# Kernel tuning notes

Hardware: AMD Instinct MI355X
Metric: run time of the kernel (lower is better)

The kernel has to match this reference:

```python
import jax, jax.numpy as jnp
import numpy as np

# Bipartite frontier sizes per layer (targets of layer i): fanouts [15,10,5] over 1024 seeds
N_TGT = (60000, 6000, 1024)


def sage_layer(x_src, n_tgt, src, dst, Wl, Wr, b):
    # PyG SAGEConv, aggr='mean', root_weight=True:
    #   out = lin_l(mean_{j in N(i)} x_j) + lin_r(x_i) + bias
    x_tgt = x_src[:n_tgt]                       # [n_tgt, d]
    msg = x_src[src]                            # gather: [E, d]
    agg = jax.ops.segment_sum(msg, dst, num_segments=n_tgt)
    cnt = jax.ops.segment_sum(jnp.ones((src.shape[0], 1), x_src.dtype), dst, num_segments=n_tgt)
    mean = agg / jnp.maximum(cnt, 1.0)          # zero-degree nodes -> 0
    return mean @ Wl + x_tgt @ Wr + b


def setup_inputs() -> dict:
    key = jax.random.key(0)
    ks = jax.random.split(key, 16)
    N0 = 900000
    E = (900000, 60000, 5120)
    dims = [(100, 256), (256, 256), (256, 47)]
    inp = {"x": jax.random.normal(ks[0], (N0, 100), dtype=jnp.float32)}
    n_src = (N0,) + N_TGT[:2]
    for i in range(3):
        inp[f"src{i}"] = jax.random.randint(ks[1 + 2 * i], (E[i],), 0, n_src[i])
        inp[f"dst{i}"] = jax.random.randint(ks[2 + 2 * i], (E[i],), 0, N_TGT[i])
    for i, (din, dout) in enumerate(dims):
        inp[f"Wl{i}"] = jax.random.normal(ks[7 + 3 * i], (din, dout), dtype=jnp.float32) * 0.05
        inp[f"Wr{i}"] = jax.random.normal(ks[8 + 3 * i], (din, dout), dtype=jnp.float32) * 0.05
        inp[f"b{i}"] = jnp.zeros((dout,), dtype=jnp.float32)
    return inp


def reference(x, src0, dst0, src1, dst1, src2, dst2,
              Wl0, Wr0, b0, Wl1, Wr1, b1, Wl2, Wr2, b2):
    srcs = (src0, src1, src2)
    dsts = (dst0, dst1, dst2)
    Wls = (Wl0, Wl1, Wl2)
    Wrs = (Wr0, Wr1, Wr2)
    bs = (b0, b1, b2)
    for i in range(3):
        x = sage_layer(x, N_TGT[i], srcs[i], dsts[i], Wls[i], Wrs[i], bs[i])
        if i != 2:
            x = jax.nn.relu(x)  # dropout is identity in eval mode
    return jax.nn.log_softmax(x, axis=-1)
```

## Files before the change

kernel.cpp:

```cpp
#include <hip/hip_runtime.h>
#include <hip/hip_bf16.h>


typedef short bf16x8 __attribute__((ext_vector_type(8)));
typedef float f32x4 __attribute__((ext_vector_type(4)));

static __device__ __forceinline__ unsigned short f2bf(float f) {
  unsigned u = __float_as_uint(f);
  unsigned r = u + 0x7FFFu + ((u >> 16) & 1u);
  return (unsigned short)(r >> 16);
}
static __device__ __forceinline__ float bf2f_lo(unsigned u) {
  return __uint_as_float(u << 16);
}
static __device__ __forceinline__ float bf2f_hi(unsigned u) {
  return __uint_as_float(u & 0xFFFF0000u);
}
static __device__ __forceinline__ unsigned packbf(float lo, float hi) {
  return ((unsigned)f2bf(hi) << 16) | (unsigned)f2bf(lo);
}

#define E0C 900000
#define E1C 60000
#define E2C 5120
#define ETC 965120
#define HB  3770

#define ROW0_OFF 0
#define ROW1_OFF 60001
#define ROW2_OFF 66002
#define CNT_OFF  67027
#define RANK_OFF 134051
#define SS0_OFF  1099171
#define SS1_OFF  1999171
#define SS2_OFF  2059171

struct TileGeom { int tin, goff, n, T; };
static __device__ __forceinline__ TileGeom tile_geom(int b) {
  TileGeom g;
  if (b < 118)      { g.tin = b;       g.goff = 0;     g.n = 60000; g.T = 118; }
  else if (b < 130) { g.tin = b - 118; g.goff = 60000; g.n = 6000;  g.T = 12; }
  else              { g.tin = b - 130; g.goff = 66000; g.n = 1024;  g.T = 2; }
  return g;
}

__global__ __launch_bounds__(256) void histrank_k(
    const int* __restrict__ d0, const int* __restrict__ d1, const int* __restrict__ d2,
    int* __restrict__ cnt, int* __restrict__ rank) {
  int t = blockIdx.x * 256 + threadIdx.x;
  if (t < E0C) {
    rank[t] = atomicAdd(&cnt[d0[t]], 1);
  } else if (t < E0C + E1C) {
    rank[t] = atomicAdd(&cnt[60000 + d1[t - E0C]], 1);
  } else if (t < ETC) {
    rank[t] = atomicAdd(&cnt[66000 + d2[t - E0C - E1C]], 1);
  }
}

__global__ __launch_bounds__(256) void scanpack_k(
    const int* __restrict__ cnt,
    int* __restrict__ row0, int* __restrict__ row1, int* __restrict__ row2,
    const float* __restrict__ Wl0, const float* __restrict__ Wr0,
    unsigned short* __restrict__ bm0,
    const float* __restrict__ Wl1, const float* __restrict__ Wr1,
    unsigned short* __restrict__ bm1) {
  const int b = blockIdx.x;
  const int tid = threadIdx.x;
  if (b < 132) {
    __shared__ int sc[256];
    const TileGeom g = tile_geom(b);
    int* row = (b < 118) ? row0 : (b < 130 ? row1 : row2);
    int p = 0;
    const int lim = g.tin * 512;
    for (int i = tid; i < lim; i += 256) p += cnt[g.goff + i];
    sc[tid] = p;
    __syncthreads();
    for (int off = 128; off; off >>= 1) {
      if (tid < off) sc[tid] += sc[tid + off];
      __syncthreads();
    }
    const int pref = sc[0];
    __syncthreads();
    const int i0 = g.tin * 512 + 2 * tid;
    const int e0 = (i0 < g.n) ? cnt[g.goff + i0] : 0;
    const int e1 = (i0 + 1 < g.n) ? cnt[g.goff + i0 + 1] : 0;
    sc[tid] = e0 + e1;
    __syncthreads();
    for (int off = 1; off < 256; off <<= 1) {
      int v = (tid >= off) ? sc[tid - off] : 0;
      __syncthreads();
      sc[tid] += v;
      __syncthreads();
    }
    const int excl = sc[tid] - (e0 + e1);
    const int o0 = pref + excl;
    const int o1 = o0 + e0;
    if (i0 < g.n) row[i0] = o0;
    if (i0 + 1 < g.n) row[i0 + 1] = o1;
    if (g.tin == g.T - 1 && tid == 255) row[g.n] = pref + sc[255];
  } else {
    int j = b - 132;
    int n = tid;
    if (j < 224) {
      int k = j;
      float v = 0.f;
      if (k < 100) v = Wl0[(size_t)k * 256 + n];
      else if (k >= 112 && k < 212) v = Wr0[(size_t)(k - 112) * 256 + n];
      bm0[(((size_t)(k >> 3) * 256) + n) * 8 + (k & 7)] = f2bf(v);
    } else {
      int k = j - 224;
      float v = (k < 256) ? Wl1[(size_t)k * 256 + n] : Wr1[(size_t)(k - 256) * 256 + n];
      bm1[(((size_t)(k >> 3) * 256) + n) * 8 + (k & 7)] = f2bf(v);
    }
  }
}

__global__ __launch_bounds__(256) void fillscatter_k(
    const int* __restrict__ d0, const int* __restrict__ d1, const int* __restrict__ d2,
    const int* __restrict__ s0, const int* __restrict__ s1, const int* __restrict__ s2,
    const int* __restrict__ row0, const int* __restrict__ row1,
    const int* __restrict__ row2, const int* __restrict__ rank,
    int* __restrict__ o0, int* __restrict__ o1, int* __restrict__ o2) {
  int t = blockIdx.x * 256 + threadIdx.x;
  if (t < E0C) {
    o0[row0[d0[t]] + rank[t]] = s0[t];
  } else if (t < E0C + E1C) {
    int e = t - E0C;
    o1[row1[d1[e]] + rank[t]] = s1[e];
  } else if (t < ETC) {
    int e = t - E0C - E1C;
    o2[row2[d2[e]] + rank[t]] = s2[e];
  }
}

__global__ __launch_bounds__(256) void gather_fused_k(
    const float* __restrict__ x, const int* __restrict__ ss,
    const int* __restrict__ rs, unsigned short* __restrict__ am, int n) {
  int idx = blockIdx.x * 256 + threadIdx.x;
  int w = idx >> 6;
  int f = idx & 63;
  if (w >= n) return;
  const int lo = rs[w];
  const int hi = rs[w + 1];
  float acc0 = 0.f, acc1 = 0.f;
  const int k1 = f + 64;
  int e = lo;
  for (; e + 4 <= hi; e += 4) {
    const float* p0 = x + (size_t)ss[e] * 100;
    const float* p1 = x + (size_t)ss[e + 1] * 100;
    const float* p2 = x + (size_t)ss[e + 2] * 100;
    const float* p3 = x + (size_t)ss[e + 3] * 100;
    acc0 += (p0[f] + p1[f]) + (p2[f] + p3[f]);
    if (k1 < 100) acc1 += (p0[k1] + p1[k1]) + (p2[k1] + p3[k1]);
  }
  for (; e < hi; ++e) {
    const float* p0 = x + (size_t)ss[e] * 100;
    acc0 += p0[f];
    if (k1 < 100) acc1 += p0[k1];
  }
  const float inv = 1.f / (float)max(hi - lo, 1);
  unsigned short* arow = am + (size_t)w * 224;
  arow[f] = f2bf(acc0 * inv);
  if (k1 < 112) arow[k1] = (k1 < 100) ? f2bf(acc1 * inv) : (unsigned short)0;
  const float* xrow = x + (size_t)w * 100;
  arow[112 + f] = f2bf(xrow[f]);
  if (k1 < 112) arow[112 + k1] = (k1 < 100) ? f2bf(xrow[k1]) : (unsigned short)0;
}

__global__ __launch_bounds__(256) void gather_mean_b16_k(
    const unsigned* __restrict__ xbu, const int* __restrict__ ss,
    const int* __restrict__ rs, unsigned* __restrict__ meanu, int n) {
  int idx = blockIdx.x * 256 + threadIdx.x;
  int w = idx >> 6;
  int f = idx & 63;
  if (w >= n) return;
  const int lo = rs[w];
  const int hi = rs[w + 1];
  float a0l = 0.f, a0h = 0.f, a1l = 0.f, a1h = 0.f;
  int e = lo;
  for (; e + 2 <= hi; e += 2) {
    const unsigned* p0 = xbu + (size_t)ss[e] * 128;
    const unsigned* p1 = xbu + (size_t)ss[e + 1] * 128;
    unsigned u0a = p0[f], u0b = p0[f + 64];
    unsigned u1a = p1[f], u1b = p1[f + 64];
    a0l += bf2f_lo(u0a) + bf2f_lo(u1a);
    a0h += bf2f_hi(u0a) + bf2f_hi(u1a);
    a1l += bf2f_lo(u0b) + bf2f_lo(u1b);
    a1h += bf2f_hi(u0b) + bf2f_hi(u1b);
  }
  for (; e < hi; ++e) {
    const unsigned* p0 = xbu + (size_t)ss[e] * 128;
    unsigned ua = p0[f], ub = p0[f + 64];
    a0l += bf2f_lo(ua); a0h += bf2f_hi(ua);
    a1l += bf2f_lo(ub); a1h += bf2f_hi(ub);
  }
  const float inv = 1.f / (float)max(hi - lo, 1);
  meanu[(size_t)w * 128 + f] = packbf(a0l * inv, a0h * inv);
  meanu[(size_t)w * 128 + f + 64] = packbf(a1l * inv, a1h * inv);
}

template <int KPAD, int C1CH, int MBLK, bool RELU, bool OUTBF>
__global__ __launch_bounds__(256) void gemm_mfma_k(
    const unsigned short* __restrict__ A1, const unsigned short* __restrict__ A2,
    const unsigned short* __restrict__ Bp, const float* __restrict__ bias,
    void* __restrict__ outv, int M, int p1, int p2) {
  constexpr int LDA = KPAD + 8;
  constexpr int CPR = KPAD / 8;
  constexpr int RT = MBLK / 16;
  constexpr int NKC = KPAD / 32;
  __shared__ unsigned short As[MBLK * LDA];

  const int row0 = blockIdx.x * MBLK;
  for (int t = threadIdx.x; t < MBLK * CPR; t += 256) {
    int r = t / CPR;
    int c = t - r * CPR;
    const unsigned short* src = (c < C1CH)
        ? (A1 + (size_t)(row0 + r) * p1 + c * 8)
        : (A2 + (size_t)(row0 + r) * p2 + (c - C1CH) * 8);
    *reinterpret_cast<uint4*>(&As[r * LDA + c * 8]) =
        *reinterpret_cast<const uint4*>(src);
  }
  __syncthreads();

  const int wid = threadIdx.x >> 6;
  const int l = threadIdx.x & 63;
  const int l15 = l & 15;
  const int lhi = l >> 4;

  f32x4 acc[RT][4];
#pragma unroll
  for (int rt = 0; rt < RT; ++rt)
#pragma unroll
    for (int ct = 0; ct < 4; ++ct) acc[rt][ct] = (f32x4){0.f, 0.f, 0.f, 0.f};

  for (int kc = 0; kc < NKC; ++kc) {
    bf16x8 a[RT], b[4];
#pragma unroll
    for (int rt = 0; rt < RT; ++rt)
      a[rt] = *reinterpret_cast<const bf16x8*>(
          &As[(rt * 16 + l15) * LDA + kc * 32 + lhi * 8]);
#pragma unroll
    for (int ct = 0; ct < 4; ++ct) {
      int n = wid * 64 + ct * 16 + l15;
      b[ct] = *reinterpret_cast<const bf16x8*>(
          Bp + ((size_t)(kc * 4 + lhi) * 256 + n) * 8);
    }
#pragma unroll
    for (int rt = 0; rt < RT; ++rt)
#pragma unroll
      for (int ct = 0; ct < 4; ++ct)
        acc[rt][ct] = __builtin_amdgcn_mfma_f32_16x16x32_bf16(a[rt], b[ct],
                                                              acc[rt][ct], 0, 0, 0);
  }

#pragma unroll
  for (int rt = 0; rt < RT; ++rt) {
#pragma unroll
    for (int ct = 0; ct < 4; ++ct) {
      int col = wid * 64 + ct * 16 + l15;
      float bv = bias[col];
#pragma unroll
      for (int r = 0; r < 4; ++r) {
        int row = row0 + rt * 16 + lhi * 4 + r;
        if (row < M) {
          float v = acc[rt][ct][r] + bv;
          if (RELU) v = fmaxf(v, 0.f);
          if (OUTBF)
            ((unsigned short*)outv)[(size_t)row * 256 + col] = f2bf(v);
          else
            ((float*)outv)[(size_t)row * 256 + col] = v;
        }
      }
    }
  }
}

__global__ __launch_bounds__(64) void final_fused_k(
    const float* __restrict__ h1, const int* __restrict__ ss,
    const int* __restrict__ rs, const float* __restrict__ Wl,
    const float* __restrict__ Wr, const float* __restrict__ bb,
    float* __restrict__ out) {
  __shared__ float sm[4][256];
  __shared__ float sx[4][256];
  const int i0 = blockIdx.x * 4;
  const int f = threadIdx.x;
#pragma unroll
  for (int r = 0; r < 4; ++r) {
    const int i = i0 + r;
    const int lo = rs[i];
    const int hi = rs[i + 1];
    float a0 = 0.f, a1 = 0.f, a2 = 0.f, a3 = 0.f;
    for (int e = lo; e < hi; ++e) {
      const float* p = h1 + (size_t)ss[e] * 256;
      a0 += p[f]; a1 += p[f + 64]; a2 += p[f + 128]; a3 += p[f + 192];
    }
    const float inv = 1.f / (float)max(hi - lo, 1);
    sm[r][f] = a0 * inv; sm[r][f + 64] = a1 * inv;
    sm[r][f + 128] = a2 * inv; sm[r][f + 192] = a3 * inv;
    const float* q = h1 + (size_t)i * 256;
    sx[r][f] = q[f]; sx[r][f + 64] = q[f + 64];
    sx[r][f + 128] = q[f + 128]; sx[r][f + 192] = q[f + 192];
  }
  __syncthreads();

  const int j = f;
  float acc[4] = {-1e30f, -1e30f, -1e30f, -1e30f};
  if (j < 47) {
    float b = bb[j];
    acc[0] = b; acc[1] = b; acc[2] = b; acc[3] = b;
    for (int k = 0; k < 256; ++k) {
      float wl = Wl[k * 47 + j];
      float wr = Wr[k * 47 + j];
#pragma unroll
      for (int r = 0; r < 4; ++r) acc[r] += sm[r][k] * wl + sx[r][k] * wr;
    }
  }
#pragma unroll
  for (int r = 0; r < 4; ++r) {
    float m = acc[r];
#pragma unroll
    for (int off = 32; off; off >>= 1) m = fmaxf(m, __shfl_xor(m, off));
    float e = (j < 47) ? expf(acc[r] - m) : 0.f;
    float s = e;
#pragma unroll
    for (int off = 32; off; off >>= 1) s += __shfl_xor(s, off);
    if (j < 47) out[(size_t)(i0 + r) * 47 + j] = acc[r] - m - logf(s);
  }
}

extern "C" void kernel_launch(void* const* d_in, const int* in_sizes, int n_in,
                              void* d_out, int out_size, void* d_ws, size_t ws_size,
                              hipStream_t stream) {
  const float* x    = (const float*)d_in[0];
  const int*   src0 = (const int*)d_in[1];
  const int*   dst0 = (const int*)d_in[2];
  const int*   src1 = (const int*)d_in[3];
  const int*   dst1 = (const int*)d_in[4];
  const int*   src2 = (const int*)d_in[5];
  const int*   dst2 = (const int*)d_in[6];
  const float* Wl0  = (const float*)d_in[7];
  const float* Wr0  = (const float*)d_in[8];
  const float* b0   = (const float*)d_in[9];
  const float* Wl1  = (const float*)d_in[10];
  const float* Wr1  = (const float*)d_in[11];
  const float* b1   = (const float*)d_in[12];
  const float* Wl2  = (const float*)d_in[13];
  const float* Wr2  = (const float*)d_in[14];
  const float* b2   = (const float*)d_in[15];
  float* out = (float*)d_out;

  const int N0 = 60000, N1 = 6000, N2 = 1024;

  char* base = (char*)d_ws;
  unsigned short* bm0  = (unsigned short*)(base);
  unsigned short* bm1  = (unsigned short*)(base + 114688);
  unsigned short* am0  = (unsigned short*)(base + 376832);
  unsigned short* h0b  = (unsigned short*)(base + 27271168);
  unsigned*       h0bu = (unsigned*)(base + 27271168);
  unsigned short* mean1= (unsigned short*)(base + 58007552);
  unsigned*       mean1u=(unsigned*)(base + 58007552);
  float* h1            = (float*)(base + 61087744);
  int* iw              = (int*)(base + 67248128);
  int* row0 = iw + ROW0_OFF;
  int* row1 = iw + ROW1_OFF;
  int* row2 = iw + ROW2_OFF;
  int* cnt  = iw + CNT_OFF;
  int* rank = iw + RANK_OFF;
  int* ss0  = iw + SS0_OFF;
  int* ss1  = iw + SS1_OFF;
  int* ss2  = iw + SS2_OFF;

  hipMemsetAsync(cnt, 0, (size_t)67024 * sizeof(int), stream);
  histrank_k<<<HB, 256, 0, stream>>>(dst0, dst1, dst2, cnt, rank);
  scanpack_k<<<132 + 736, 256, 0, stream>>>(cnt, row0, row1, row2,
                                            Wl0, Wr0, bm0, Wl1, Wr1, bm1);
  fillscatter_k<<<HB, 256, 0, stream>>>(dst0, dst1, dst2, src0, src1, src2,
                                        row0, row1, row2, rank, ss0, ss1, ss2);

  gather_fused_k<<<(N0 * 64 + 255) / 256, 256, 0, stream>>>(x, ss0, row0, am0, N0);
  gemm_mfma_k<224, 28, 64, true, true><<<(N0 + 63) / 64, 256, 0, stream>>>(
      am0, am0, bm0, b0, (void*)h0b, N0, 224, 224);

  gather_mean_b16_k<<<(N1 * 64 + 255) / 256, 256, 0, stream>>>(
      h0bu, ss1, row1, mean1u, N1);
  gemm_mfma_k<512, 32, 32, true, false><<<(N1 + 31) / 32, 256, 0, stream>>>(
      mean1, h0b, bm1, b1, (void*)h1, N1, 256, 256);

  final_fused_k<<<N2 / 4, 64, 0, stream>>>(h1, ss2, row2, Wl2, Wr2, b2, out);
}
```

Before: 277.1 us.

## Stage layer-0 GEMM output through LDS for coalesced stores; widen final kernel

The templated MFMA GEMM is split into two specialised kernels. The layer-0 GEMM now writes its bf16 ReLU tile into shared memory (reusing the A-tile buffer with a wider stride) and then stores full rows to global memory with 16-byte vector writes, replacing scattered 2-byte stores. The final layer kernel moves from 64-thread blocks looping over 4 rows to 256-thread blocks with one wave per target row, giving more parallelism for the gather and projection. The cost is two extra barriers and a larger shared-memory footprint in gemm0, which may reduce occupancy.

```diff
diff --git a/kernel.cpp b/kernel.cpp
--- a/kernel.cpp
+++ b/kernel.cpp
@@ -199,26 +199,19 @@
   meanu[(size_t)w * 128 + f + 64] = packbf(a1l * inv, a1h * inv);
 }
 
-template <int KPAD, int C1CH, int MBLK, bool RELU, bool OUTBF>
-__global__ __launch_bounds__(256) void gemm_mfma_k(
-    const unsigned short* __restrict__ A1, const unsigned short* __restrict__ A2,
-    const unsigned short* __restrict__ Bp, const float* __restrict__ bias,
-    void* __restrict__ outv, int M, int p1, int p2) {
-  constexpr int LDA = KPAD + 8;
-  constexpr int CPR = KPAD / 8;
-  constexpr int RT = MBLK / 16;
-  constexpr int NKC = KPAD / 32;
-  __shared__ unsigned short As[MBLK * LDA];
-
-  const int row0 = blockIdx.x * MBLK;
-  for (int t = threadIdx.x; t < MBLK * CPR; t += 256) {
-    int r = t / CPR;
-    int c = t - r * CPR;
-    const unsigned short* src = (c < C1CH)
-        ? (A1 + (size_t)(row0 + r) * p1 + c * 8)
-        : (A2 + (size_t)(row0 + r) * p2 + (c - C1CH) * 8);
-    *reinterpret_cast<uint4*>(&As[r * LDA + c * 8]) =
-        *reinterpret_cast<const uint4*>(src);
+__global__ __launch_bounds__(256) void gemm0_k(
+    const unsigned short* __restrict__ A, const unsigned short* __restrict__ Bp,
+    const float* __restrict__ bias, unsigned short* __restrict__ h0b, int M) {
+  constexpr int LDA = 232;
+  constexpr int LDC = 264;
+  __shared__ unsigned short Sh[64 * LDC];
+
+  const int row0 = blockIdx.x * 64;
+  for (int t = threadIdx.x; t < 64 * 28; t += 256) {
+    int r = t / 28;
+    int c = t - r * 28;
+    *reinterpret_cast<uint4*>(&Sh[r * LDA + c * 8]) =
+        *reinterpret_cast<const uint4*>(A + (size_t)(row0 + r) * 224 + c * 8);
   }
   __syncthreads();
 
@@ -227,18 +220,18 @@
   const int l15 = l & 15;
   const int lhi = l >> 4;
 
-  f32x4 acc[RT][4];
-#pragma unroll
-  for (int rt = 0; rt < RT; ++rt)
+  f32x4 acc[4][4];
+#pragma unroll
+  for (int rt = 0; rt < 4; ++rt)
 #pragma unroll
     for (int ct = 0; ct < 4; ++ct) acc[rt][ct] = (f32x4){0.f, 0.f, 0.f, 0.f};
 
-  for (int kc = 0; kc < NKC; ++kc) {
-    bf16x8 a[RT], b[4];
-#pragma unroll
-    for (int rt = 0; rt < RT; ++rt)
+  for (int kc = 0; kc < 7; ++kc) {
+    bf16x8 a[4], b[4];
+#pragma unroll
+    for (int rt = 0; rt < 4; ++rt)
       a[rt] = *reinterpret_cast<const bf16x8*>(
-          &As[(rt * 16 + l15) * LDA + kc * 32 + lhi * 8]);
+          &Sh[(rt * 16 + l15) * LDA + kc * 32 + lhi * 8]);
 #pragma unroll
     for (int ct = 0; ct < 4; ++ct) {
       int n = wid * 64 + ct * 16 + l15;
@@ -246,86 +239,148 @@
           Bp + ((size_t)(kc * 4 + lhi) * 256 + n) * 8);
     }
 #pragma unroll
-    for (int rt = 0; rt < RT; ++rt)
+    for (int rt = 0; rt < 4; ++rt)
 #pragma unroll
       for (int ct = 0; ct < 4; ++ct)
         acc[rt][ct] = __builtin_amdgcn_mfma_f32_16x16x32_bf16(a[rt], b[ct],
                                                               acc[rt][ct], 0, 0, 0);
   }
-
-#pragma unroll
-  for (int rt = 0; rt < RT; ++rt) {
+  __syncthreads();
+
+#pragma unroll
+  for (int rt = 0; rt < 4; ++rt) {
 #pragma unroll
     for (int ct = 0; ct < 4; ++ct) {
       int col = wid * 64 + ct * 16 + l15;
       float bv = bias[col];
 #pragma unroll
       for (int r = 0; r < 4; ++r) {
+        int rr = rt * 16 + lhi * 4 + r;
+        Sh[rr * LDC + col] = f2bf(fmaxf(acc[rt][ct][r] + bv, 0.f));
+      }
+    }
+  }
+  __syncthreads();
+
+  const int mrem = M - row0;
+  for (int t = threadIdx.x; t < 64 * 32; t += 256) {
+    int r = t >> 5;
+    int c = t & 31;
+    if (r < mrem) {
+      *reinterpret_cast<uint4*>(h0b + (size_t)(row0 + r) * 256 + c * 8) =
+          *reinterpret_cast<const uint4*>(&Sh[r * LDC + c * 8]);
+    }
+  }
+}
+
+__global__ __launch_bounds__(256) void gemm1_k(
+    const unsigned short* __restrict__ A1, const unsigned short* __restrict__ A2,
+    const unsigned short* __restrict__ Bp, const float* __restrict__ bias,
+    float* __restrict__ h1, int M) {
+  constexpr int LDA = 520;
+  __shared__ unsigned short As[32 * LDA];
+
+  const int row0 = blockIdx.x * 32;
+  for (int t = threadIdx.x; t < 32 * 64; t += 256) {
+    int r = t >> 6;
+    int c = t & 63;
+    const unsigned short* src = (c < 32)
+        ? (A1 + (size_t)(row0 + r) * 256 + c * 8)
+        : (A2 + (size_t)(row0 + r) * 256 + (c - 32) * 8);
+    *reinterpret_cast<uint4*>(&As[r * LDA + c * 8]) =
+        *reinterpret_cast<const uint4*>(src);
+  }
+  __syncthreads();
+
+  const int wid = threadIdx.x >> 6;
+  const int l = threadIdx.x & 63;
+  const int l15 = l & 15;
+  const int lhi = l >> 4;
+
+  f32x4 acc[2][4];
+#pragma unroll
+  for (int rt = 0; rt < 2; ++rt)
+#pragma unroll
+    for (int ct = 0; ct < 4; ++ct) acc[rt][ct] = (f32x4){0.f, 0.f, 0.f, 0.f};
+
+  for (int kc = 0; kc < 16; ++kc) {
+    bf16x8 a[2], b[4];
+#pragma unroll
+    for (int rt = 0; rt < 2; ++rt)
+      a[rt] = *reinterpret_cast<const bf16x8*>(
+          &As[(rt * 16 + l15) * LDA + kc * 32 + lhi * 8]);
+#pragma unroll
+    for (int ct = 0; ct < 4; ++ct) {
+      int n = wid * 64 + ct * 16 + l15;
+      b[ct] = *reinterpret_cast<const bf16x8*>(
+          Bp + ((size_t)(kc * 4 + lhi) * 256 + n) * 8);
+    }
+#pragma unroll
+    for (int rt = 0; rt < 2; ++rt)
+#pragma unroll
+      for (int ct = 0; ct < 4; ++ct)
+        acc[rt][ct] = __builtin_amdgcn_mfma_f32_16x16x32_bf16(a[rt], b[ct],
+                                                              acc[rt][ct], 0, 0, 0);
+  }
+
+#pragma unroll
+  for (int rt = 0; rt < 2; ++rt) {
+#pragma unroll
+    for (int ct = 0; ct < 4; ++ct) {
+      int col = wid * 64 + ct * 16 + l15;
+      float bv = bias[col];
+#pragma unroll
+      for (int r = 0; r < 4; ++r) {
         int row = row0 + rt * 16 + lhi * 4 + r;
-        if (row < M) {
-          float v = acc[rt][ct][r] + bv;
-          if (RELU) v = fmaxf(v, 0.f);
-          if (OUTBF)
-            ((unsigned short*)outv)[(size_t)row * 256 + col] = f2bf(v);
-          else
-            ((float*)outv)[(size_t)row * 256 + col] = v;
-        }
+        if (row < M)
+          h1[(size_t)row * 256 + col] = fmaxf(acc[rt][ct][r] + bv, 0.f);
       }
     }
   }
 }
 
-__global__ __launch_bounds__(64) void final_fused_k(
+__global__ __launch_bounds__(256) void final_fused_k(
     const float* __restrict__ h1, const int* __restrict__ ss,
     const int* __restrict__ rs, const float* __restrict__ Wl,
     const float* __restrict__ Wr, const float* __restrict__ bb,
     float* __restrict__ out) {
   __shared__ float sm[4][256];
   __shared__ float sx[4][256];
-  const int i0 = blockIdx.x * 4;
-  const int f = threadIdx.x;
-#pragma unroll
-  for (int r = 0; r < 4; ++r) {
-    const int i = i0 + r;
-    const int lo = rs[i];
-    const int hi = rs[i + 1];
-    float a0 = 0.f, a1 = 0.f, a2 = 0.f, a3 = 0.f;
-    for (int e = lo; e < hi; ++e) {
-      const float* p = h1 + (size_t)ss[e] * 256;
-      a0 += p[f]; a1 += p[f + 64]; a2 += p[f + 128]; a3 += p[f + 192];
-    }
-    const float inv = 1.f / (float)max(hi - lo, 1);
-    sm[r][f] = a0 * inv; sm[r][f + 64] = a1 * inv;
-    sm[r][f + 128] = a2 * inv; sm[r][f + 192] = a3 * inv;
-    const float* q = h1 + (size_t)i * 256;
-    sx[r][f] = q[f]; sx[r][f + 64] = q[f + 64];
-    sx[r][f + 128] = q[f + 128]; sx[r][f + 192] = q[f + 192];
-  }
-  __syncthreads();
-
-  const int j = f;
-  float acc[4] = {-1e30f, -1e30f, -1e30f, -1e30f};
-  if (j < 47) {
-    float b = bb[j];
-    acc[0] = b; acc[1] = b; acc[2] = b; acc[3] = b;
+  const int w = threadIdx.x >> 6;
+  const int f = threadIdx.x & 63;
+  const int i = blockIdx.x * 4 + w;
+
+  const int lo = rs[i];
+  const int hi = rs[i + 1];
+  float a0 = 0.f, a1 = 0.f, a2 = 0.f, a3 = 0.f;
+  for (int e = lo; e < hi; ++e) {
+    const float* p = h1 + (size_t)ss[e] * 256;
+    a0 += p[f]; a1 += p[f + 64]; a2 += p[f + 128]; a3 += p[f + 192];
+  }
+  const float inv = 1.f / (float)max(hi - lo, 1);
+  sm[w][f] = a0 * inv; sm[w][f + 64] = a1 * inv;
+  sm[w][f + 128] = a2 * inv; sm[w][f + 192] = a3 * inv;
+  const float* q = h1 + (size_t)i * 256;
+  sx[w][f] = q[f]; sx[w][f + 64] = q[f + 64];
+  sx[w][f + 128] = q[f + 128]; sx[w][f + 192] = q[f + 192];
+
+  float acc = -1e30f;
+  if (f < 47) {
+    float b = bb[f];
+    float a = b;
     for (int k = 0; k < 256; ++k) {
-      float wl = Wl[k * 47 + j];
-      float wr = Wr[k * 47 + j];
-#pragma unroll
-      for (int r = 0; r < 4; ++r) acc[r] += sm[r][k] * wl + sx[r][k] * wr;
-    }
-  }
-#pragma unroll
-  for (int r = 0; r < 4; ++r) {
-    float m = acc[r];
-#pragma unroll
-    for (int off = 32; off; off >>= 1) m = fmaxf(m, __shfl_xor(m, off));
-    float e = (j < 47) ? expf(acc[r] - m) : 0.f;
-    float s = e;
-#pragma unroll
-    for (int off = 32; off; off >>= 1) s += __shfl_xor(s, off);
-    if (j < 47) out[(size_t)(i0 + r) * 47 + j] = acc[r] - m - logf(s);
-  }
+      a += sm[w][k] * Wl[k * 47 + f] + sx[w][k] * Wr[k * 47 + f];
+    }
+    acc = a;
+  }
+  float m = acc;
+#pragma unroll
+  for (int off = 32; off; off >>= 1) m = fmaxf(m, __shfl_xor(m, off));
+  float e2 = (f < 47) ? expf(acc - m) : 0.f;
+  float s = e2;
+#pragma unroll
+  for (int off = 32; off; off >>= 1) s += __shfl_xor(s, off);
+  if (f < 47) out[(size_t)i * 47 + f] = acc - m - logf(s);
 }
 
 extern "C" void kernel_launch(void* const* d_in, const int* in_sizes, int n_in,
@@ -378,13 +433,11 @@
                                         row0, row1, row2, rank, ss0, ss1, ss2);
 
   gather_fused_k<<<(N0 * 64 + 255) / 256, 256, 0, stream>>>(x, ss0, row0, am0, N0);
-  gemm_mfma_k<224, 28, 64, true, true><<<(N0 + 63) / 64, 256, 0, stream>>>(
-      am0, am0, bm0, b0, (void*)h0b, N0, 224, 224);
+  gemm0_k<<<(N0 + 63) / 64, 256, 0, stream>>>(am0, bm0, b0, h0b, N0);
 
   gather_mean_b16_k<<<(N1 * 64 + 255) / 256, 256, 0, stream>>>(
       h0bu, ss1, row1, mean1u, N1);
-  gemm_mfma_k<512, 32, 32, true, false><<<(N1 + 31) / 32, 256, 0, stream>>>(
-      mean1, h0b, bm1, b1, (void*)h1, N1, 256, 256);
-
-  final_fused_k<<<N2 / 4, 64, 0, stream>>>(h1, ss2, row2, Wl2, Wr2, b2, out);
-}
+  gemm1_k<<<(N1 + 31) / 32, 256, 0, stream>>>(mean1, h0b, bm1, b1, h1, N1);
+
+  final_fused_k<<<N2 / 4, 256, 0, stream>>>(h1, ss2, row2, Wl2, Wr2, b2, out);
+}
```

Measured after the change: 255.9 us. -7.6%, faster.
